# Optimization experiments

Measured on AMD Instinct MI355X. Metric: run time of the kernel, lower is better.

Reference implementation:

```python
import jax, jax.numpy as jnp
import numpy as np

B, SQ, SK = 2, 2048, 2048
D_MODEL, N_HEADS = 1024, 16
D_HEAD = D_MODEL // N_HEADS
LN_EPS = 1e-5


def _ln(x, w, b):
    # per-head LayerNorm over last dim (d_head)
    mu = jnp.mean(x, axis=-1, keepdims=True)
    var = jnp.mean(jnp.square(x - mu), axis=-1, keepdims=True)
    return (x - mu) * jax.lax.rsqrt(var + LN_EPS) * w + b


def setup_inputs() -> dict:
    key = jax.random.key(0)
    ks = jax.random.split(key, 8)
    sd = 1.0 / np.sqrt(D_MODEL)
    so = 1.0 / np.sqrt(D_HEAD)
    return {
        "x_q": jax.random.normal(ks[0], (B, SQ, D_MODEL), jnp.float32),
        "x_kv": jax.random.normal(ks[1], (B, SK, D_MODEL), jnp.float32),
        "mask": jnp.tril(jnp.ones((SQ, SK), dtype=bool)),  # causal
        "W_Q": jax.random.normal(ks[2], (N_HEADS, D_MODEL, D_HEAD), jnp.float32) * sd,
        "W_K": jax.random.normal(ks[3], (N_HEADS, D_MODEL, D_HEAD), jnp.float32) * sd,
        "W_V": jax.random.normal(ks[4], (N_HEADS, D_MODEL, D_HEAD), jnp.float32) * sd,
        "W_O": jax.random.normal(ks[5], (N_HEADS, D_HEAD, D_MODEL), jnp.float32) * so,
        "b_Q": jnp.zeros((N_HEADS, D_HEAD), jnp.float32),
        "b_K": jnp.zeros((N_HEADS, D_HEAD), jnp.float32),
        "b_V": jnp.zeros((N_HEADS, D_HEAD), jnp.float32),
        "b_O": jnp.zeros((D_MODEL,), jnp.float32),
        "ln1_w": jnp.ones((D_HEAD,), jnp.float32),
        "ln1_b": jnp.zeros((D_HEAD,), jnp.float32),
        "ln2_w": jnp.ones((D_HEAD,), jnp.float32),
        "ln2_b": jnp.zeros((D_HEAD,), jnp.float32),
    }


def reference(x_q, x_kv, mask, W_Q, W_K, W_V, W_O, b_Q, b_K, b_V, b_O,
              ln1_w, ln1_b, ln2_w, ln2_b):
    # QKV projections: b s d, n d h -> b s n h
    q = jnp.einsum('bsd,ndh->bsnh', x_q, W_Q) + b_Q
    k = jnp.einsum('bsd,ndh->bsnh', x_kv, W_K) + b_K
    v = jnp.einsum('bsd,ndh->bsnh', x_kv, W_V) + b_V
    # QK-norm (ln_first=False, rope=None -> just apply LN after projections)
    q = _ln(q, ln1_w, ln1_b)
    k = _ln(k, ln2_w, ln2_b)
    # NOTE: no 1/sqrt(d_head) scaling, matching the original module
    att = jnp.einsum('bqnh,bknh->bnqk', q, k)
    att = jnp.where(mask, att, -jnp.inf)
    probas = jax.nn.softmax(att, axis=-1)
    z = jnp.einsum('bnqk,bknh->bqnh', probas, v)
    out = jnp.einsum('bqnh,nhd->bqd', z, W_O) + b_O
    return (out, k, v)
```

## Files before the change

kernel.cpp:

```cpp
#include <hip/hip_runtime.h>
#include <hip/hip_bf16.h>

#define B_   2
#define SQ_  2048
#define DM_  1024
#define NH_  16
#define DH_  64

typedef __attribute__((ext_vector_type(8))) short          bf16x8;
typedef __attribute__((ext_vector_type(8))) unsigned short u16x8;
typedef __attribute__((ext_vector_type(4))) float          f32x4;

__device__ __forceinline__ unsigned short f2bf(float f) {
    union { __hip_bfloat16 h; unsigned short u; } c;
    c.h = __float2bfloat16(f);
    return c.u;
}
__device__ __forceinline__ float gsum16(float v) {
    v += __shfl_xor(v, 1);
    v += __shfl_xor(v, 2);
    v += __shfl_xor(v, 4);
    v += __shfl_xor(v, 8);
    return v;
}

__global__ __launch_bounds__(256) void prep_all(
    const float* __restrict__ W_Q, const float* __restrict__ W_K,
    const float* __restrict__ W_V, const float* __restrict__ W_O,
    const float* __restrict__ x_q, const float* __restrict__ x_kv,
    unsigned short* __restrict__ WTq, unsigned short* __restrict__ WTkv,
    unsigned short* __restrict__ WTo,
    unsigned short* __restrict__ xqbf, unsigned short* __restrict__ xkvbf)
{
    const int bid = blockIdx.x, tid = threadIdx.x;
    if (bid >= 1024) {
        const int cid = bid - 1024;
        const float* src = (cid < 256) ? x_q : x_kv;
        unsigned short* dst = (cid < 256) ? xqbf : xkvbf;
        const size_t base = (size_t)(cid & 255) * 16384 + tid * 4;
#pragma unroll
        for (int i = 0; i < 16; ++i) {
            const float4 v = *(const float4*)(src + base + i * 1024);
            ushort4 o;
            o.x = f2bf(v.x); o.y = f2bf(v.y); o.z = f2bf(v.z); o.w = f2bf(v.w);
            *(ushort4*)(dst + base + i * 1024) = o;
        }
        return;
    }
    __shared__ float t[64][65];
    const float* src; unsigned short* dst; int R, C, r0, c0;
    if (bid < 768) {
        const int which = bid >> 8, rem = bid & 255;
        const int rblk = rem & 15, zz = rem >> 4;
        src = (which == 0) ? W_Q : (which == 1) ? W_K : W_V;
        dst = (which == 0) ? WTq : (which == 1) ? WTkv : (WTkv + (1u << 20));
        src += (size_t)65536 * zz;
        dst += (size_t)65536 * zz;
        R = 1024; C = 64; r0 = rblk * 64; c0 = 0;
    } else {
        const int rem = bid - 768;
        src = W_O; dst = WTo; R = 1024; C = 1024;
        r0 = (rem & 15) * 64; c0 = (rem >> 4) * 64;
    }
    const int lr = tid >> 6, lc = tid & 63;
#pragma unroll
    for (int i = 0; i < 16; ++i)
        t[lr + i * 4][lc] = src[(size_t)(r0 + lr + i * 4) * C + c0 + lc];
    __syncthreads();
#pragma unroll
    for (int i = 0; i < 16; ++i)
        dst[(size_t)(c0 + lr + i * 4) * R + r0 + lc] = f2bf(t[lc][lr + i * 4]);
}

template <int TN, int MODE>
__device__ __forceinline__ void gemm_body(
    unsigned short (*__restrict__ As)[72], unsigned short (*__restrict__ Bs)[72],
    int bx, int by, const unsigned short* __restrict__ Abf,
    const unsigned short* __restrict__ WT,
    const float* __restrict__ biasK, const float* __restrict__ biasV,
    const float* __restrict__ lnw, const float* __restrict__ lnb,
    float* __restrict__ Cf, float* __restrict__ Cf2,
    unsigned short* __restrict__ Cb, unsigned short* __restrict__ CbT, int tid)
{
    constexpr int MI = (TN == 128) ? 4 : 2;
    constexpr int BP = TN / 64;

    const int m0 = by * 128;
    const int c0 = bx * TN;

    const int srow = tid >> 2;
    const int skc  = (tid & 3) * 16;

    u16x8 ba[2][2];
    u16x8 bb[BP][2];

    const int wid = tid >> 6, lane = tid & 63;
    const int wm = (TN == 128) ? (wid >> 1) * 64 : wid * 32;
    const int wn = (TN == 128) ? (wid & 1) * 64 : 0;
    const int l15 = lane & 15, qd = lane >> 4;

    const f32x4 zero4 = {0.f, 0.f, 0.f, 0.f};
    f32x4 acc[MI][4];
#pragma unroll
    for (int mi = 0; mi < MI; ++mi)
#pragma unroll
        for (int ni = 0; ni < 4; ++ni) acc[mi][ni] = zero4;

#define LOAD_AB(kb)                                                             \
    {                                                                           \
        const size_t kof = (size_t)(kb) * 64 + skc;                             \
        for (int p = 0; p < 2; ++p) {                                           \
            const unsigned short* s =                                           \
                Abf + (size_t)(m0 + srow + p * 64) * 1024 + kof;                \
            ba[p][0] = *(const u16x8*)(s + 0);                                  \
            ba[p][1] = *(const u16x8*)(s + 8);                                  \
        }                                                                       \
        for (int p = 0; p < BP; ++p) {                                          \
            const unsigned short* s =                                           \
                WT + (size_t)(c0 + srow + p * 64) * 1024 + kof;                 \
            bb[p][0] = *(const u16x8*)(s + 0);                                  \
            bb[p][1] = *(const u16x8*)(s + 8);                                  \
        }                                                                       \
    }

    LOAD_AB(0)
    for (int kb = 0; kb < 16; ++kb) {
        __syncthreads();
#pragma unroll
        for (int p = 0; p < 2; ++p) {
            *(u16x8*)&As[srow + p * 64][skc + 0] = ba[p][0];
            *(u16x8*)&As[srow + p * 64][skc + 8] = ba[p][1];
        }
#pragma unroll
        for (int p = 0; p < BP; ++p) {
            *(u16x8*)&Bs[srow + p * 64][skc + 0] = bb[p][0];
            *(u16x8*)&Bs[srow + p * 64][skc + 8] = bb[p][1];
        }
        __syncthreads();
        if (kb < 15) LOAD_AB(kb + 1)
#pragma unroll
        for (int ks = 0; ks < 2; ++ks) {
            bf16x8 af[MI], bfr[4];
#pragma unroll
            for (int mi = 0; mi < MI; ++mi)
                af[mi] = *(const bf16x8*)&As[wm + mi * 16 + l15][ks * 32 + qd * 8];
#pragma unroll
            for (int ni = 0; ni < 4; ++ni)
                bfr[ni] = *(const bf16x8*)&Bs[wn + ni * 16 + l15][ks * 32 + qd * 8];
#pragma unroll
            for (int mi = 0; mi < MI; ++mi)
#pragma unroll
                for (int ni = 0; ni < 4; ++ni)
                    acc[mi][ni] = __builtin_amdgcn_mfma_f32_16x16x32_bf16(
                        af[mi], bfr[ni], acc[mi][ni], 0, 0, 0);
        }
    }
#undef LOAD_AB

    const float* bias = (MODE == 1 && c0 >= 1024) ? biasV : biasK;
    float bv[4];
#pragma unroll
    for (int ni = 0; ni < 4; ++ni) bv[ni] = bias[(c0 + wn + ni * 16 + l15) & 1023];
#pragma unroll
    for (int mi = 0; mi < MI; ++mi)
#pragma unroll
        for (int ni = 0; ni < 4; ++ni)
#pragma unroll
            for (int r = 0; r < 4; ++r) acc[mi][ni][r] += bv[ni];

    if constexpr (MODE != 2) {
        const bool doLN = (MODE == 0) || (c0 < 1024);
        if (doLN) {
            float w4[4], lb4[4];
#pragma unroll
            for (int ni = 0; ni < 4; ++ni) {
                w4[ni]  = lnw[ni * 16 + l15];
                lb4[ni] = lnb[ni * 16 + l15];
            }
#pragma unroll
            for (int mi = 0; mi < MI; ++mi)
#pragma unroll
                for (int r = 0; r < 4; ++r) {
                    float s1 = acc[mi][0][r] + acc[mi][1][r] + acc[mi][2][r] + acc[mi][3][r];
                    const float mu = gsum16(s1) * (1.0f / 64.0f);
                    float s2 = acc[mi][0][r] * acc[mi][0][r] + acc[mi][1][r] * acc[mi][1][r]
                             + acc[mi][2][r] * acc[mi][2][r] + acc[mi][3][r] * acc[mi][3][r];
                    const float var = gsum16(s2) * (1.0f / 64.0f) - mu * mu;
                    const float rstd = rsqrtf(var + 1e-5f);
#pragma unroll
                    for (int ni = 0; ni < 4; ++ni)
                        acc[mi][ni][r] = (acc[mi][ni][r] - mu) * rstd * w4[ni] + lb4[ni];
                }
        }
    }

    if constexpr (MODE == 0) {
#pragma unroll
        for (int mi = 0; mi < MI; ++mi)
#pragma unroll
            for (int r = 0; r < 4; ++r) {
                const size_t grow = m0 + wm + mi * 16 + qd * 4 + r;
#pragma unroll
                for (int ni = 0; ni < 4; ++ni)
                    Cb[grow * 1024 + c0 + wn + ni * 16 + l15] = f2bf(acc[mi][ni][r]);
            }
    } else if constexpr (MODE == 2) {
#pragma unroll
        for (int mi = 0; mi < MI; ++mi)
#pragma unroll
            for (int r = 0; r < 4; ++r) {
                const size_t grow = m0 + wm + mi * 16 + qd * 4 + r;
#pragma unroll
                for (int ni = 0; ni < 4; ++ni)
                    Cf[grow * 1024 + c0 + wn + ni * 16 + l15] = acc[mi][ni][r];
            }
    } else {
        if (c0 < 1024) {
#pragma unroll
            for (int mi = 0; mi < MI; ++mi)
#pragma unroll
                for (int r = 0; r < 4; ++r) {
                    const size_t grow = m0 + wm + mi * 16 + qd * 4 + r;
#pragma unroll
                    for (int ni = 0; ni < 4; ++ni) {
                        const int gcol = c0 + wn + ni * 16 + l15;
                        Cf[grow * 1024 + gcol] = acc[mi][ni][r];
                        Cb[grow * 1024 + gcol] = f2bf(acc[mi][ni][r]);
                    }
                }
        } else {
#pragma unroll
            for (int mi = 0; mi < MI; ++mi) {
                const int growb = m0 + wm + mi * 16 + qd * 4;
                const int bb_ = growb >> 11, ss = growb & 2047;
#pragma unroll
                for (int ni = 0; ni < 4; ++ni) {
                    const int gv = c0 - 1024 + wn + ni * 16 + l15;
                    const int hh = gv >> 6, dd = gv & 63;
#pragma unroll
                    for (int r = 0; r < 4; ++r)
                        Cf2[(size_t)(growb + r) * 1024 + gv] = acc[mi][ni][r];
                    ushort4 w;
                    w.x = f2bf(acc[mi][ni][0]); w.y = f2bf(acc[mi][ni][1]);
                    w.z = f2bf(acc[mi][ni][2]); w.w = f2bf(acc[mi][ni][3]);
                    *(ushort4*)&CbT[(((size_t)bb_ * NH_ + hh) * DH_ + dd) * SQ_ + ss] = w;
                }
            }
        }
    }
}

__global__ __launch_bounds__(256) void qkv_fused(
    const unsigned short* __restrict__ xqbf, const unsigned short* __restrict__ xkvbf,
    const unsigned short* __restrict__ WTq, const unsigned short* __restrict__ WTkv,
    const float* __restrict__ b_Q, const float* __restrict__ b_K,
    const float* __restrict__ b_V,
    const float* __restrict__ ln1w, const float* __restrict__ ln1b,
    const float* __restrict__ ln2w, const float* __restrict__ ln2b,
    float* __restrict__ kout, float* __restrict__ vout,
    unsigned short* __restrict__ qz, unsigned short* __restrict__ kbf,
    unsigned short* __restrict__ vbfT)
{
    __shared__ __align__(16) unsigned short As[128][72];
    __shared__ __align__(16) unsigned short Bs[128][72];
    const int bid = blockIdx.x, tid = threadIdx.x;
    if (bid < 512) {
        gemm_body<128, 1>(As, Bs, bid & 15, bid >> 4, xkvbf, WTkv, b_K, b_V,
                          ln2w, ln2b, kout, vout, kbf, vbfT, tid);
    } else {
        const int b2 = bid - 512;
        gemm_body<128, 0>(As, Bs, b2 & 7, b2 >> 3, xqbf, WTq, b_Q, nullptr,
                          ln1w, ln1b, nullptr, nullptr, qz, nullptr, tid);
    }
}

__global__ __launch_bounds__(256) void o_gemm(
    const unsigned short* __restrict__ zbf, const unsigned short* __restrict__ WTo,
    const float* __restrict__ b_O, float* __restrict__ out)
{
    __shared__ __align__(16) unsigned short As[128][72];
    __shared__ __align__(16) unsigned short Bs[64][72];
    gemm_body<64, 2>(As, Bs, blockIdx.x, blockIdx.y, zbf, WTo, b_O, nullptr,
                     nullptr, nullptr, out, nullptr, nullptr, nullptr, threadIdx.x);
}

__global__ __launch_bounds__(256) void attn_mfma(
    unsigned short* __restrict__ qz, const unsigned short* __restrict__ kbf,
    const unsigned short* __restrict__ vbfT)
{
    __shared__ __align__(16) unsigned short Ks[64][72];
    __shared__ __align__(16) unsigned short VsT[64][72];
    __shared__ __align__(16) unsigned short Ps[64][72];

    const int tid = threadIdx.x;
    const int h = blockIdx.y, b = blockIdx.z;
    const int wid = tid >> 6, lane = tid & 63;
    const int l15 = lane & 15, qd = lane >> 4;
    const int srow = tid >> 2, scol = (tid & 3) * 16;

    const size_t kbase = (size_t)b * SQ_ * DM_ + (size_t)h * DH_;
    const size_t vbase = ((size_t)b * NH_ + h) * DH_ * (size_t)SQ_;
    const f32x4 zero4 = {0.f, 0.f, 0.f, 0.f};

    for (int pass = 0; pass < 2; ++pass) {
        const int qt = pass ? blockIdx.x : 31 - blockIdx.x;

        bf16x8 qf[2];
        {
            const unsigned short* qp =
                qz + kbase + (size_t)(qt * 64 + wid * 16 + l15) * DM_ + qd * 8;
            qf[0] = *(const bf16x8*)(qp);
            qf[1] = *(const bf16x8*)(qp + 32);
        }

        f32x4 z[4];
#pragma unroll
        for (int ni = 0; ni < 4; ++ni) z[ni] = zero4;
        float m_i = -3.0e38f, l_i = 0.f;

        u16x8 kr0, kr1, vr0, vr1;
        {
            const unsigned short* ks = kbf + kbase + (size_t)srow * DM_ + scol;
            kr0 = *(const u16x8*)(ks);
            kr1 = *(const u16x8*)(ks + 8);
            const unsigned short* vs = vbfT + vbase + (size_t)srow * SQ_ + scol;
            vr0 = *(const u16x8*)(vs);
            vr1 = *(const u16x8*)(vs + 8);
        }

        for (int kt = 0; kt <= qt; ++kt) {
            __syncthreads();
            *(u16x8*)&Ks[srow][scol + 0]  = kr0;
            *(u16x8*)&Ks[srow][scol + 8]  = kr1;
            *(u16x8*)&VsT[srow][scol + 0] = vr0;
            *(u16x8*)&VsT[srow][scol + 8] = vr1;
            __syncthreads();
            if (kt < qt) {
                const unsigned short* ks =
                    kbf + kbase + (size_t)((kt + 1) * 64 + srow) * DM_ + scol;
                kr0 = *(const u16x8*)(ks);
                kr1 = *(const u16x8*)(ks + 8);
                const unsigned short* vs =
                    vbfT + vbase + (size_t)srow * SQ_ + (kt + 1) * 64 + scol;
                vr0 = *(const u16x8*)(vs);
                vr1 = *(const u16x8*)(vs + 8);
            }

            f32x4 s[4];
#pragma unroll
            for (int mi = 0; mi < 4; ++mi) s[mi] = zero4;
#pragma unroll
            for (int ks2 = 0; ks2 < 2; ++ks2)
#pragma unroll
                for (int mi = 0; mi < 4; ++mi) {
                    const bf16x8 af = *(const bf16x8*)&Ks[mi * 16 + l15][ks2 * 32 + qd * 8];
                    s[mi] = __builtin_amdgcn_mfma_f32_16x16x32_bf16(af, qf[ks2], s[mi], 0, 0, 0);
                }

            if (kt == qt) {
#pragma unroll
                for (int mi = 0; mi < 4; ++mi)
#pragma unroll
                    for (int r = 0; r < 4; ++r)
                        if (mi * 16 + qd * 4 + r > wid * 16 + l15) s[mi][r] = -3.0e38f;
            }

            float mloc = -3.0e38f;
#pragma unroll
            for (int mi = 0; mi < 4; ++mi)
#pragma unroll
                for (int r = 0; r < 4; ++r) mloc = fmaxf(mloc, s[mi][r]);
            mloc = fmaxf(mloc, __shfl_xor(mloc, 16));
            mloc = fmaxf(mloc, __shfl_xor(mloc, 32));
            const float mn = fmaxf(m_i, mloc);
            const float alpha = __expf(m_i - mn);
            float rs = 0.f;
#pragma unroll
            for (int mi = 0; mi < 4; ++mi)
#pragma unroll
                for (int r = 0; r < 4; ++r) {
                    const float e = __expf(s[mi][r] - mn);
                    s[mi][r] = e;
                    rs += e;
                }
            rs += __shfl_xor(rs, 16);
            rs += __shfl_xor(rs, 32);
            l_i = l_i * alpha + rs;
            m_i = mn;

#pragma unroll
            for (int mi = 0; mi < 4; ++mi) {
                ushort4 w;
                w.x = f2bf(s[mi][0]); w.y = f2bf(s[mi][1]);
                w.z = f2bf(s[mi][2]); w.w = f2bf(s[mi][3]);
                *(ushort4*)&Ps[wid * 16 + l15][mi * 16 + qd * 4] = w;
            }

#pragma unroll
            for (int r = 0; r < 4; ++r) {
                const float ar = __shfl(alpha, qd * 4 + r);
#pragma unroll
                for (int ni = 0; ni < 4; ++ni) z[ni][r] *= ar;
            }

#pragma unroll
            for (int ks2 = 0; ks2 < 2; ++ks2) {
                const bf16x8 ap = *(const bf16x8*)&Ps[wid * 16 + l15][ks2 * 32 + qd * 8];
#pragma unroll
                for (int ni = 0; ni < 4; ++ni) {
                    const bf16x8 bv = *(const bf16x8*)&VsT[ni * 16 + l15][ks2 * 32 + qd * 8];
                    z[ni] = __builtin_amdgcn_mfma_f32_16x16x32_bf16(ap, bv, z[ni], 0, 0, 0);
                }
            }
        }

        const float linv = 1.0f / l_i;
#pragma unroll
        for (int r = 0; r < 4; ++r) {
            const float lr_ = __shfl(linv, qd * 4 + r);
            const size_t row = (size_t)qt * 64 + wid * 16 + qd * 4 + r;
#pragma unroll
            for (int ni = 0; ni < 4; ++ni)
                qz[kbase + row * DM_ + ni * 16 + l15] = f2bf(z[ni][r] * lr_);
        }
    }
}

extern "C" void kernel_launch(void* const* d_in, const int* in_sizes, int n_in,
                              void* d_out, int out_size, void* d_ws, size_t ws_size,
                              hipStream_t stream)
{
    const float* x_q  = (const float*)d_in[0];
    const float* x_kv = (const float*)d_in[1];
    const float* W_Q  = (const float*)d_in[3];
    const float* W_K  = (const float*)d_in[4];
    const float* W_V  = (const float*)d_in[5];
    const float* W_O  = (const float*)d_in[6];
    const float* b_Q  = (const float*)d_in[7];
    const float* b_K  = (const float*)d_in[8];
    const float* b_V  = (const float*)d_in[9];
    const float* b_O  = (const float*)d_in[10];
    const float* ln1w = (const float*)d_in[11];
    const float* ln1b = (const float*)d_in[12];
    const float* ln2w = (const float*)d_in[13];
    const float* ln2b = (const float*)d_in[14];

    const size_t NTOK = (size_t)B_ * SQ_;
    float* out  = (float*)d_out;
    float* kout = out + NTOK * DM_;
    float* vout = kout + NTOK * DM_;

    unsigned short* xqbf  = (unsigned short*)out;
    unsigned short* xkvbf = xqbf + (1u << 22);

    unsigned short* wsu  = (unsigned short*)d_ws;
    unsigned short* WTq  = wsu;
    unsigned short* WTkv = WTq + (1u << 20);
    unsigned short* WTo  = WTkv + (2u << 20);
    unsigned short* qz   = WTo + (1u << 20);
    unsigned short* kbf  = qz + (1u << 22);
    unsigned short* vbfT = kbf + (1u << 22);

    prep_all<<<1536, 256, 0, stream>>>(W_Q, W_K, W_V, W_O, x_q, x_kv,
                                       WTq, WTkv, WTo, xqbf, xkvbf);

    qkv_fused<<<768, 256, 0, stream>>>(xqbf, xkvbf, WTq, WTkv, b_Q, b_K, b_V,
                                       ln1w, ln1b, ln2w, ln2b,
                                       kout, vout, qz, kbf, vbfT);

    attn_mfma<<<dim3(16, NH_, B_), 256, 0, stream>>>(qz, kbf, vbfT);

    o_gemm<<<dim3(16, 32), 256, 0, stream>>>(qz, WTo, b_O, out);
}
```

Before: 247.5 us.

## Use direct global-to-LDS loads in GEMMs and split attention into one q-tile per block

```diff
diff --git a/kernel.cpp b/kernel.cpp
--- a/kernel.cpp
+++ b/kernel.cpp
@@ -22,6 +22,13 @@
     v += __shfl_xor(v, 4);
     v += __shfl_xor(v, 8);
     return v;
+}
+
+__device__ __forceinline__ void gll16(const unsigned short* g, unsigned short* l) {
+    __builtin_amdgcn_global_load_lds(
+        (const __attribute__((address_space(1))) unsigned int*)g,
+        (__attribute__((address_space(3))) unsigned int*)l,
+        16, 0, 0);
 }
 
 __global__ __launch_bounds__(256) void prep_all(
@@ -74,7 +81,7 @@
 
 template <int TN, int MODE>
 __device__ __forceinline__ void gemm_body(
-    unsigned short (*__restrict__ As)[72], unsigned short (*__restrict__ Bs)[72],
+    unsigned short (*__restrict__ As)[64], unsigned short (*__restrict__ Bs)[64],
     int bx, int by, const unsigned short* __restrict__ Abf,
     const unsigned short* __restrict__ WT,
     const float* __restrict__ biasK, const float* __restrict__ biasV,
@@ -88,17 +95,17 @@
     const int m0 = by * 128;
     const int c0 = bx * TN;
 
-    const int srow = tid >> 2;
-    const int skc  = (tid & 3) * 16;
-
-    u16x8 ba[2][2];
-    u16x8 bb[BP][2];
-
     const int wid = tid >> 6, lane = tid & 63;
     const int wm = (TN == 128) ? (wid >> 1) * 64 : wid * 32;
     const int wn = (TN == 128) ? (wid & 1) * 64 : 0;
     const int l15 = lane & 15, qd = lane >> 4;
 
+    const int srow = tid >> 3, scol = (tid & 7) * 8;
+    const unsigned short* Ag = Abf + (size_t)(m0 + srow) * 1024 + scol;
+    const unsigned short* Bg = WT  + (size_t)(c0 + srow) * 1024 + scol;
+    unsigned short* Al = &As[srow][scol];
+    unsigned short* Bl = &Bs[srow][scol];
+
     const f32x4 zero4 = {0.f, 0.f, 0.f, 0.f};
     f32x4 acc[MI][4];
 #pragma unroll
@@ -106,38 +113,16 @@
 #pragma unroll
         for (int ni = 0; ni < 4; ++ni) acc[mi][ni] = zero4;
 
-#define LOAD_AB(kb)                                                             \
-    {                                                                           \
-        const size_t kof = (size_t)(kb) * 64 + skc;                             \
-        for (int p = 0; p < 2; ++p) {                                           \
-            const unsigned short* s =                                           \
-                Abf + (size_t)(m0 + srow + p * 64) * 1024 + kof;                \
-            ba[p][0] = *(const u16x8*)(s + 0);                                  \
-            ba[p][1] = *(const u16x8*)(s + 8);                                  \
-        }                                                                       \
-        for (int p = 0; p < BP; ++p) {                                          \
-            const unsigned short* s =                                           \
-                WT + (size_t)(c0 + srow + p * 64) * 1024 + kof;                 \
-            bb[p][0] = *(const u16x8*)(s + 0);                                  \
-            bb[p][1] = *(const u16x8*)(s + 8);                                  \
-        }                                                                       \
-    }
-
-    LOAD_AB(0)
     for (int kb = 0; kb < 16; ++kb) {
+        const size_t kof = (size_t)kb * 64;
         __syncthreads();
 #pragma unroll
-        for (int p = 0; p < 2; ++p) {
-            *(u16x8*)&As[srow + p * 64][skc + 0] = ba[p][0];
-            *(u16x8*)&As[srow + p * 64][skc + 8] = ba[p][1];
-        }
-#pragma unroll
-        for (int p = 0; p < BP; ++p) {
-            *(u16x8*)&Bs[srow + p * 64][skc + 0] = bb[p][0];
-            *(u16x8*)&Bs[srow + p * 64][skc + 8] = bb[p][1];
-        }
+        for (int j = 0; j < 4; ++j)
+            gll16(Ag + (size_t)j * 32 * 1024 + kof, Al + j * 32 * 64);
+#pragma unroll
+        for (int j = 0; j < 2 * BP; ++j)
+            gll16(Bg + (size_t)j * 32 * 1024 + kof, Bl + j * 32 * 64);
         __syncthreads();
-        if (kb < 15) LOAD_AB(kb + 1)
 #pragma unroll
         for (int ks = 0; ks < 2; ++ks) {
             bf16x8 af[MI], bfr[4];
@@ -155,7 +140,6 @@
                         af[mi], bfr[ni], acc[mi][ni], 0, 0, 0);
         }
     }
-#undef LOAD_AB
 
     const float* bias = (MODE == 1 && c0 >= 1024) ? biasV : biasK;
     float bv[4];
@@ -261,8 +245,8 @@
     unsigned short* __restrict__ qz, unsigned short* __restrict__ kbf,
     unsigned short* __restrict__ vbfT)
 {
-    __shared__ __align__(16) unsigned short As[128][72];
-    __shared__ __align__(16) unsigned short Bs[128][72];
+    __shared__ __align__(16) unsigned short As[128][64];
+    __shared__ __align__(16) unsigned short Bs[128][64];
     const int bid = blockIdx.x, tid = threadIdx.x;
     if (bid < 512) {
         gemm_body<128, 1>(As, Bs, bid & 15, bid >> 4, xkvbf, WTkv, b_K, b_V,
@@ -278,8 +262,8 @@
     const unsigned short* __restrict__ zbf, const unsigned short* __restrict__ WTo,
     const float* __restrict__ b_O, float* __restrict__ out)
 {
-    __shared__ __align__(16) unsigned short As[128][72];
-    __shared__ __align__(16) unsigned short Bs[64][72];
+    __shared__ __align__(16) unsigned short As[128][64];
+    __shared__ __align__(16) unsigned short Bs[64][64];
     gemm_body<64, 2>(As, Bs, blockIdx.x, blockIdx.y, zbf, WTo, b_O, nullptr,
                      nullptr, nullptr, out, nullptr, nullptr, nullptr, threadIdx.x);
 }
@@ -302,127 +286,125 @@
     const size_t vbase = ((size_t)b * NH_ + h) * DH_ * (size_t)SQ_;
     const f32x4 zero4 = {0.f, 0.f, 0.f, 0.f};
 
-    for (int pass = 0; pass < 2; ++pass) {
-        const int qt = pass ? blockIdx.x : 31 - blockIdx.x;
-
-        bf16x8 qf[2];
-        {
-            const unsigned short* qp =
-                qz + kbase + (size_t)(qt * 64 + wid * 16 + l15) * DM_ + qd * 8;
-            qf[0] = *(const bf16x8*)(qp);
-            qf[1] = *(const bf16x8*)(qp + 32);
-        }
-
-        f32x4 z[4];
-#pragma unroll
-        for (int ni = 0; ni < 4; ++ni) z[ni] = zero4;
-        float m_i = -3.0e38f, l_i = 0.f;
-
-        u16x8 kr0, kr1, vr0, vr1;
-        {
-            const unsigned short* ks = kbf + kbase + (size_t)srow * DM_ + scol;
+    const int qt = 31 - (int)blockIdx.x;
+
+    bf16x8 qf[2];
+    {
+        const unsigned short* qp =
+            qz + kbase + (size_t)(qt * 64 + wid * 16 + l15) * DM_ + qd * 8;
+        qf[0] = *(const bf16x8*)(qp);
+        qf[1] = *(const bf16x8*)(qp + 32);
+    }
+
+    f32x4 z[4];
+#pragma unroll
+    for (int ni = 0; ni < 4; ++ni) z[ni] = zero4;
+    float m_i = -3.0e38f, l_i = 0.f;
+
+    u16x8 kr0, kr1, vr0, vr1;
+    {
+        const unsigned short* ks = kbf + kbase + (size_t)srow * DM_ + scol;
+        kr0 = *(const u16x8*)(ks);
+        kr1 = *(const u16x8*)(ks + 8);
+        const unsigned short* vs = vbfT + vbase + (size_t)srow * SQ_ + scol;
+        vr0 = *(const u16x8*)(vs);
+        vr1 = *(const u16x8*)(vs + 8);
+    }
+
+    for (int kt = 0; kt <= qt; ++kt) {
+        __syncthreads();
+        *(u16x8*)&Ks[srow][scol + 0]  = kr0;
+        *(u16x8*)&Ks[srow][scol + 8]  = kr1;
+        *(u16x8*)&VsT[srow][scol + 0] = vr0;
+        *(u16x8*)&VsT[srow][scol + 8] = vr1;
+        __syncthreads();
+        if (kt < qt) {
+            const unsigned short* ks =
+                kbf + kbase + (size_t)((kt + 1) * 64 + srow) * DM_ + scol;
             kr0 = *(const u16x8*)(ks);
             kr1 = *(const u16x8*)(ks + 8);
-            const unsigned short* vs = vbfT + vbase + (size_t)srow * SQ_ + scol;
+            const unsigned short* vs =
+                vbfT + vbase + (size_t)srow * SQ_ + (kt + 1) * 64 + scol;
             vr0 = *(const u16x8*)(vs);
             vr1 = *(const u16x8*)(vs + 8);
         }
 
-        for (int kt = 0; kt <= qt; ++kt) {
-            __syncthreads();
-            *(u16x8*)&Ks[srow][scol + 0]  = kr0;
-            *(u16x8*)&Ks[srow][scol + 8]  = kr1;
-            *(u16x8*)&VsT[srow][scol + 0] = vr0;
-            *(u16x8*)&VsT[srow][scol + 8] = vr1;
-            __syncthreads();
-            if (kt < qt) {
-                const unsigned short* ks =
-                    kbf + kbase + (size_t)((kt + 1) * 64 + srow) * DM_ + scol;
-                kr0 = *(const u16x8*)(ks);
-                kr1 = *(const u16x8*)(ks + 8);
-                const unsigned short* vs =
-                    vbfT + vbase + (size_t)srow * SQ_ + (kt + 1) * 64 + scol;
-                vr0 = *(const u16x8*)(vs);
-                vr1 = *(const u16x8*)(vs + 8);
-            }
-
-            f32x4 s[4];
-#pragma unroll
-            for (int mi = 0; mi < 4; ++mi) s[mi] = zero4;
-#pragma unroll
-            for (int ks2 = 0; ks2 < 2; ++ks2)
-#pragma unroll
-                for (int mi = 0; mi < 4; ++mi) {
-                    const bf16x8 af = *(const bf16x8*)&Ks[mi * 16 + l15][ks2 * 32 + qd * 8];
-                    s[mi] = __builtin_amdgcn_mfma_f32_16x16x32_bf16(af, qf[ks2], s[mi], 0, 0, 0);
-                }
-
-            if (kt == qt) {
-#pragma unroll
-                for (int mi = 0; mi < 4; ++mi)
-#pragma unroll
-                    for (int r = 0; r < 4; ++r)
-                        if (mi * 16 + qd * 4 + r > wid * 16 + l15) s[mi][r] = -3.0e38f;
-            }
-
-            float mloc = -3.0e38f;
+        f32x4 s[4];
+#pragma unroll
+        for (int mi = 0; mi < 4; ++mi) s[mi] = zero4;
+#pragma unroll
+        for (int ks2 = 0; ks2 < 2; ++ks2)
+#pragma unroll
+            for (int mi = 0; mi < 4; ++mi) {
+                const bf16x8 af = *(const bf16x8*)&Ks[mi * 16 + l15][ks2 * 32 + qd * 8];
+                s[mi] = __builtin_amdgcn_mfma_f32_16x16x32_bf16(af, qf[ks2], s[mi], 0, 0, 0);
+            }
+
+        if (kt == qt) {
 #pragma unroll
             for (int mi = 0; mi < 4; ++mi)
 #pragma unroll
-                for (int r = 0; r < 4; ++r) mloc = fmaxf(mloc, s[mi][r]);
-            mloc = fmaxf(mloc, __shfl_xor(mloc, 16));
-            mloc = fmaxf(mloc, __shfl_xor(mloc, 32));
-            const float mn = fmaxf(m_i, mloc);
-            const float alpha = __expf(m_i - mn);
-            float rs = 0.f;
-#pragma unroll
-            for (int mi = 0; mi < 4; ++mi)
-#pragma unroll
-                for (int r = 0; r < 4; ++r) {
-                    const float e = __expf(s[mi][r] - mn);
-                    s[mi][r] = e;
-                    rs += e;
-                }
-            rs += __shfl_xor(rs, 16);
-            rs += __shfl_xor(rs, 32);
-            l_i = l_i * alpha + rs;
-            m_i = mn;
-
-#pragma unroll
-            for (int mi = 0; mi < 4; ++mi) {
-                ushort4 w;
-                w.x = f2bf(s[mi][0]); w.y = f2bf(s[mi][1]);
-                w.z = f2bf(s[mi][2]); w.w = f2bf(s[mi][3]);
-                *(ushort4*)&Ps[wid * 16 + l15][mi * 16 + qd * 4] = w;
-            }
-
+                for (int r = 0; r < 4; ++r)
+                    if (mi * 16 + qd * 4 + r > wid * 16 + l15) s[mi][r] = -3.0e38f;
+        }
+
+        float mloc = -3.0e38f;
+#pragma unroll
+        for (int mi = 0; mi < 4; ++mi)
+#pragma unroll
+            for (int r = 0; r < 4; ++r) mloc = fmaxf(mloc, s[mi][r]);
+        mloc = fmaxf(mloc, __shfl_xor(mloc, 16));
+        mloc = fmaxf(mloc, __shfl_xor(mloc, 32));
+        const float mn = fmaxf(m_i, mloc);
+        const float alpha = __expf(m_i - mn);
+        float rs = 0.f;
+#pragma unroll
+        for (int mi = 0; mi < 4; ++mi)
 #pragma unroll
             for (int r = 0; r < 4; ++r) {
-                const float ar = __shfl(alpha, qd * 4 + r);
-#pragma unroll
-                for (int ni = 0; ni < 4; ++ni) z[ni][r] *= ar;
-            }
-
-#pragma unroll
-            for (int ks2 = 0; ks2 < 2; ++ks2) {
-                const bf16x8 ap = *(const bf16x8*)&Ps[wid * 16 + l15][ks2 * 32 + qd * 8];
-#pragma unroll
-                for (int ni = 0; ni < 4; ++ni) {
-                    const bf16x8 bv = *(const bf16x8*)&VsT[ni * 16 + l15][ks2 * 32 + qd * 8];
-                    z[ni] = __builtin_amdgcn_mfma_f32_16x16x32_bf16(ap, bv, z[ni], 0, 0, 0);
-                }
-            }
-        }
-
-        const float linv = 1.0f / l_i;
+                const float e = __expf(s[mi][r] - mn);
+                s[mi][r] = e;
+                rs += e;
+            }
+        rs += __shfl_xor(rs, 16);
+        rs += __shfl_xor(rs, 32);
+        l_i = l_i * alpha + rs;
+        m_i = mn;
+
+#pragma unroll
+        for (int mi = 0; mi < 4; ++mi) {
+            ushort4 w;
+            w.x = f2bf(s[mi][0]); w.y = f2bf(s[mi][1]);
+            w.z = f2bf(s[mi][2]); w.w = f2bf(s[mi][3]);
+            *(ushort4*)&Ps[wid * 16 + l15][mi * 16 + qd * 4] = w;
+        }
+
 #pragma unroll
         for (int r = 0; r < 4; ++r) {
-            const float lr_ = __shfl(linv, qd * 4 + r);
-            const size_t row = (size_t)qt * 64 + wid * 16 + qd * 4 + r;
-#pragma unroll
-            for (int ni = 0; ni < 4; ++ni)
-                qz[kbase + row * DM_ + ni * 16 + l15] = f2bf(z[ni][r] * lr_);
-        }
+            const float ar = __shfl(alpha, qd * 4 + r);
+#pragma unroll
+            for (int ni = 0; ni < 4; ++ni) z[ni][r] *= ar;
+        }
+
+#pragma unroll
+        for (int ks2 = 0; ks2 < 2; ++ks2) {
+            const bf16x8 ap = *(const bf16x8*)&Ps[wid * 16 + l15][ks2 * 32 + qd * 8];
+#pragma unroll
+            for (int ni = 0; ni < 4; ++ni) {
+                const bf16x8 bv = *(const bf16x8*)&VsT[ni * 16 + l15][ks2 * 32 + qd * 8];
+                z[ni] = __builtin_amdgcn_mfma_f32_16x16x32_bf16(ap, bv, z[ni], 0, 0, 0);
+            }
+        }
+    }
+
+    const float linv = 1.0f / l_i;
+#pragma unroll
+    for (int r = 0; r < 4; ++r) {
+        const float lr_ = __shfl(linv, qd * 4 + r);
+        const size_t row = (size_t)qt * 64 + wid * 16 + qd * 4 + r;
+#pragma unroll
+        for (int ni = 0; ni < 4; ++ni)
+            qz[kbase + row * DM_ + ni * 16 + l15] = f2bf(z[ni][r] * lr_);
     }
 }
 
@@ -468,7 +450,7 @@
                                        ln1w, ln1b, ln2w, ln2b,
                                        kout, vout, qz, kbf, vbfT);
 
-    attn_mfma<<<dim3(16, NH_, B_), 256, 0, stream>>>(qz, kbf, vbfT);
+    attn_mfma<<<dim3(32, NH_, B_), 256, 0, stream>>>(qz, kbf, vbfT);
 
     o_gemm<<<dim3(16, 32), 256, 0, stream>>>(qz, WTo, b_O, out);
 }
```

Measured after the change: 281.5 us. 1.14x slower.
